# Kernel tuning notes

Measured on AMD Instinct MI355X. Metric: run time of the kernel, lower is better.

## Reference

```python
import jax, jax.numpy as jnp
import numpy as np

N_HEADS = 16
HEAD_DIM = 64
THRESHOLD = 0.5
TAU = 12.5
N_FHN_STEPS = 2


def fhn_imex_step(v, w, I, a, b, dt, tau):
    # IMEX step of FitzHugh-Nagumo dynamics:
    #   explicit update for v (nonlinear), implicit for w (linear in w)
    #   dv/dt = v - v^3/3 - w + I
    #   dw/dt = (v + a - b*w) / tau
    v_new = v + dt * (v - v ** 3 / 3.0 - w + I)
    w_new = (w + (dt / tau) * (v_new + a)) / (1.0 + (dt / tau) * b)
    return v_new, w_new


def setup_inputs() -> dict:
    key = jax.random.key(0)
    k1, k2, k3 = jax.random.split(key, 3)
    B, T, D = 2, 2048, 1024
    x = jax.random.normal(k1, (B, T, D), dtype=jnp.float32)
    Wqkv = jax.random.normal(k2, (3 * D, D), dtype=jnp.float32) * 0.02
    Wout = jax.random.normal(k3, (D, D), dtype=jnp.float32) * 0.02
    a = jnp.float32(0.7)
    b = jnp.float32(0.8)
    dt = jnp.float32(1.0)
    return {"x": x, "Wqkv": Wqkv, "Wout": Wout, "a": a, "b": b, "dt": dt}


def reference(x, Wqkv, Wout, a, b, dt):
    B, T, D = x.shape
    H, hd = N_HEADS, HEAD_DIM
    qkv = x @ Wqkv.T                              # (B, T, 3D)
    qkv = qkv.reshape(B, T, 3, H, hd)             # 'b t (three h d)'
    q = qkv[:, :, 0].transpose(0, 2, 1, 3)        # (B, H, T, hd)
    k = qkv[:, :, 1].transpose(0, 2, 1, 3)
    v = qkv[:, :, 2].transpose(0, 2, 1, 3)

    scores = jnp.einsum('bhtd,bhsd->bhts', q, k) / np.sqrt(hd).astype(np.float32)
    causal = jnp.triu(jnp.ones((T, T), dtype=bool), k=1)
    scores = jnp.where(causal[None, None], -jnp.inf, scores)
    attn_probs = jax.nn.softmax(scores, axis=-1)  # (B, H, T, T); dropout=0 -> identity

    attn_energy = attn_probs.sum(axis=-1)                              # (B, H, T)
    stim_scale = jnp.maximum(jnp.abs(attn_energy).max(axis=-1, keepdims=True), 1e-6)
    stimulus_normed = attn_energy / stim_scale
    threshold_gate = jax.nn.sigmoid((jnp.abs(attn_energy) - THRESHOLD) * 10.0)
    I = stimulus_normed * (0.1 + 0.9 * threshold_gate)                 # (B, H, T)
    I = jnp.broadcast_to(I[..., None], (B, H, T, hd))                  # expand to head_dim

    v_state = jnp.zeros_like(I)
    w_state = jnp.zeros_like(I)
    for _ in range(N_FHN_STEPS):
        v_state, w_state = fhn_imex_step(v_state, w_state, I, a, b, dt, TAU)

    fhn_gate = jax.nn.sigmoid(v_state.mean(axis=-1))[..., None]        # (B, H, T, 1)
    attn_probs = attn_probs * (0.5 + 0.5 * fhn_gate)
    attn_probs = attn_probs / (attn_probs.sum(axis=-1, keepdims=True) + 1e-8)

    out = jnp.einsum('bhts,bhsd->bhtd', attn_probs, v)                 # (B, H, T, hd)
    out = out.transpose(0, 2, 1, 3).reshape(B, T, D)
    out = out @ Wout.T
    return out
```

## Files before the change

### kernel.cpp

```cpp
#include <hip/hip_runtime.h>

typedef unsigned short u16;
typedef __attribute__((ext_vector_type(8))) short bf16x8;
typedef __attribute__((ext_vector_type(4))) float f32x4;
typedef __attribute__((ext_vector_type(4))) unsigned short u16x4;
typedef __attribute__((ext_vector_type(4))) unsigned int u32x4;

__device__ __forceinline__ u16 f2bf(float f) {
    unsigned int u = __builtin_bit_cast(unsigned int, f);
    u += 0x7fffu + ((u >> 16) & 1u);
    return (u16)(u >> 16);
}

__device__ __forceinline__ float bf2f(u16 b) {
    unsigned int u = ((unsigned int)b) << 16;
    return __builtin_bit_cast(float, u);
}

__device__ __forceinline__ unsigned int cvt_pk_bf16(float lo, float hi) {
    unsigned int r;
    asm("v_cvt_pk_bf16_f32 %0, %1, %2" : "=v"(r) : "v"(lo), "v"(hi));
    return r;
}

__device__ __forceinline__ void gload_lds16(const u16* g, const u16* l) {
    __builtin_amdgcn_global_load_lds((const __attribute__((address_space(1))) void*)g,
                                     (__attribute__((address_space(3))) void*)l,
                                     16, 0, 0);
}

__global__ __launch_bounds__(256) void cvt3_f32_bf16(const float* __restrict__ a, u16* __restrict__ ab, int na4,
                                                     const float* __restrict__ b, u16* __restrict__ bb, int nb4,
                                                     const float* __restrict__ c, u16* __restrict__ cb, int nc4) {
    const int stride = gridDim.x * blockDim.x;
    int i0 = blockIdx.x * blockDim.x + threadIdx.x;
    for (int i = i0; i < na4; i += stride) {
        float4 v = reinterpret_cast<const float4*>(a)[i];
        u16x4 o = { f2bf(v.x), f2bf(v.y), f2bf(v.z), f2bf(v.w) };
        reinterpret_cast<u16x4*>(ab)[i] = o;
    }
    for (int i = i0; i < nb4; i += stride) {
        float4 v = reinterpret_cast<const float4*>(b)[i];
        u16x4 o = { f2bf(v.x), f2bf(v.y), f2bf(v.z), f2bf(v.w) };
        reinterpret_cast<u16x4*>(bb)[i] = o;
    }
    for (int i = i0; i < nc4; i += stride) {
        float4 v = reinterpret_cast<const float4*>(c)[i];
        u16x4 o = { f2bf(v.x), f2bf(v.y), f2bf(v.z), f2bf(v.w) };
        reinterpret_cast<u16x4*>(cb)[i] = o;
    }
}

template <int BM, int BN, typename OutT>
__global__ __launch_bounds__(256) void gemm_bt(const u16* __restrict__ A, const u16* __restrict__ B,
                                               OutT* __restrict__ C, int M, int N, int K) {
    __shared__ u16 ldsA[BM * 64];
    __shared__ u16 ldsB[BN * 64];
    constexpr int RA = BM * 8 / 256;
    constexpr int RB = BN * 8 / 256;
    constexpr int MF = BM / 32;
    constexpr int NF = BN / 32;
    const int tid = threadIdx.x;
    const int lane = tid & 63;
    const int wid = tid >> 6;
    const int wm = wid >> 1, wn = wid & 1;
    const int lq = lane & 15, lg = lane >> 4;

    const int nbn = N / BN;
    const int id = blockIdx.x;
    const int idp = (id & 7) * ((int)gridDim.x >> 3) + (id >> 3);
    const int bm = (idp / nbn) * BM;
    const int bn = (idp % nbn) * BN;

    const u16* aSrc[RA];
    const u16* bSrc[RB];
    int dstOffA[RA], dstOffB[RB];
#pragma unroll
    for (int j = 0; j < RA; ++j) {
        int item = j * 256 + tid;
        aSrc[j] = A + (size_t)(bm + (item >> 3)) * K + (item & 7) * 8;
        dstOffA[j] = (j * 256 + (tid & ~63)) * 16;
    }
#pragma unroll
    for (int j = 0; j < RB; ++j) {
        int item = j * 256 + tid;
        bSrc[j] = B + (size_t)(bn + (item >> 3)) * K + (item & 7) * 8;
        dstOffB[j] = (j * 256 + (tid & ~63)) * 16;
    }

    f32x4 acc[MF][NF] = {};
    for (int k0 = 0; k0 < K; k0 += 64) {
        if (k0) __syncthreads();
#pragma unroll
        for (int j = 0; j < RA; ++j) {
            gload_lds16(aSrc[j], (const u16*)((const char*)ldsA + dstOffA[j]));
            aSrc[j] += 64;
        }
#pragma unroll
        for (int j = 0; j < RB; ++j) {
            gload_lds16(bSrc[j], (const u16*)((const char*)ldsB + dstOffB[j]));
            bSrc[j] += 64;
        }
        __syncthreads();
#pragma unroll
        for (int kk = 0; kk < 2; ++kk) {
            bf16x8 af[MF], bfr[NF];
#pragma unroll
            for (int m = 0; m < MF; ++m) {
                int row = wm * (BM / 2) + m * 16 + lq;
                af[m] = *(const bf16x8*)((const char*)ldsA + row * 128 + kk * 64 + lg * 16);
            }
#pragma unroll
            for (int n = 0; n < NF; ++n) {
                int row = wn * (BN / 2) + n * 16 + lq;
                bfr[n] = *(const bf16x8*)((const char*)ldsB + row * 128 + kk * 64 + lg * 16);
            }
#pragma unroll
            for (int m = 0; m < MF; ++m)
#pragma unroll
                for (int n = 0; n < NF; ++n)
                    acc[m][n] = __builtin_amdgcn_mfma_f32_16x16x32_bf16(af[m], bfr[n], acc[m][n], 0, 0, 0);
        }
    }

#pragma unroll
    for (int m = 0; m < MF; ++m) {
#pragma unroll
        for (int n = 0; n < NF; ++n) {
#pragma unroll
            for (int r = 0; r < 4; ++r) {
                int row = bm + wm * (BM / 2) + m * 16 + lg * 4 + r;
                int col = bn + wn * (BN / 2) + n * 16 + lq;
                float v = acc[m][n][r];
                if constexpr (sizeof(OutT) == 2)
                    C[(size_t)row * N + col] = (OutT)f2bf(v);
                else
                    C[(size_t)row * N + col] = (OutT)v;
            }
        }
    }
}

__global__ __launch_bounds__(256) void transpose_v(const u16* __restrict__ qkv, u16* __restrict__ vt) {
    __shared__ u16 tile[64][72];
    const int tb = blockIdx.x * 64;
    const int bh = blockIdx.y;
    const int b = bh >> 4, h = bh & 15;
    const u16* src = qkv + ((size_t)(b * 2048 + tb)) * 3072 + 2048 + h * 64;
    const int tid = threadIdx.x;
#pragma unroll
    for (int p = 0; p < 2; ++p) {
        int item = p * 256 + tid;
        int t = item >> 3, c = item & 7;
        bf16x8 v = *(const bf16x8*)(src + (size_t)t * 3072 + c * 8);
        *(bf16x8*)(&tile[t][c * 8]) = v;
    }
    __syncthreads();
    u16* dst = vt + ((size_t)bh * 64) * 2048 + tb;
#pragma unroll
    for (int p = 0; p < 2; ++p) {
        int item = p * 256 + tid;
        int d = item >> 3, tc = item & 7;
        bf16x8 o;
#pragma unroll
        for (int j = 0; j < 8; ++j) o[j] = (short)tile[tc * 8 + j][d];
        *(bf16x8*)(dst + (size_t)d * 2048 + tc * 8) = o;
    }
}

__global__ __launch_bounds__(256, 4) void fhn_attn(const u16* __restrict__ qkv, const u16* __restrict__ vt,
                                                   u16* __restrict__ attno,
                                                   u16* __restrict__ pO, float* __restrict__ pML) {
    __shared__ u16 kvbuf[2][2][64 * 64];
    const int id = blockIdx.x;
    const int xcd = id & 7;
    const int u = id >> 3;
    const int bh = xcd * 4 + (u & 3);
    const int unit = u >> 2;
    int qt, jb0, jb1, sidx;
    bool split;
    if (unit < 32) {
        qt = 31 - (unit >> 1);
        sidx = unit & 1;
        split = true;
        int n = qt + 1, hh = (n + 1) >> 1;
        jb0 = sidx ? hh : 0;
        jb1 = sidx ? n : hh;
    } else {
        qt = 47 - unit;
        sidx = 0;
        split = false;
        jb0 = 0;
        jb1 = qt + 1;
    }
    const int b = bh >> 4, h = bh & 15;
    const int tid = threadIdx.x;
    const int w = tid >> 6;
    const int lane = tid & 63;
    const int lq = lane & 15, lg = lane >> 4;
    const int qlo = qt * 64 + w * 16;
    const int tq = qlo + lq;

    bf16x8 qf[2];
    {
        const u16* qrow = qkv + ((size_t)(b * 2048 + tq)) * 3072 + h * 64;
        qf[0] = *(const bf16x8*)(qrow + lg * 8);
        qf[1] = *(const bf16x8*)(qrow + 32 + lg * 8);
#pragma unroll
        for (int kk = 0; kk < 2; ++kk)
#pragma unroll
            for (int j = 0; j < 8; ++j)
                qf[kk][j] = (short)f2bf(bf2f((u16)qf[kk][j]) * 0.1803368801f);
    }

    const int it0 = tid, it1 = 256 + tid;
    const int r0 = it0 >> 3, g0 = (it0 & 7) ^ (r0 & 7);
    const int r1 = it1 >> 3, g1 = (it1 & 7) ^ (r1 & 7);
    const int pr0 = (((r0 >> 4) & 1) << 5) | ((r0 & 12) << 1) | (((r0 >> 5) & 1) << 2) | (r0 & 3);
    const int pr1 = (((r1 >> 4) & 1) << 5) | ((r1 & 12) << 1) | (((r1 >> 5) & 1) << 2) | (r1 & 3);
    const u16* kS0 = qkv + ((size_t)(b * 2048 + jb0 * 64 + pr0)) * 3072 + 1024 + h * 64 + g0 * 8;
    const u16* kS1 = qkv + ((size_t)(b * 2048 + jb0 * 64 + pr1)) * 3072 + 1024 + h * 64 + g1 * 8;
    const u16* vS0 = vt + ((size_t)bh * 64 + r0) * 2048 + jb0 * 64 + g0 * 8;
    const u16* vS1 = vt + ((size_t)bh * 64 + r1) * 2048 + jb0 * 64 + g1 * 8;
    const int d0 = (it0 & ~63) * 8;
    const int d1 = (it1 & ~63) * 8;

#define STAGE(buf)                                            \
    do {                                                      \
        gload_lds16(kS0, &kvbuf[buf][0][d0]);                 \
        gload_lds16(kS1, &kvbuf[buf][0][d1]);                 \
        gload_lds16(vS0, &kvbuf[buf][1][d0]);                 \
        gload_lds16(vS1, &kvbuf[buf][1][d1]);                 \
        kS0 += 64 * 3072; kS1 += 64 * 3072;                   \
        vS0 += 64; vS1 += 64;                                 \
    } while (0)

    float m_run = -1e30f;
    f32x4 lacc = { 0.f, 0.f, 0.f, 0.f };
    f32x4 oacc[4] = {};
    int cur = 0;

    STAGE(0);

    for (int jb = jb0; jb < jb1; ++jb) {
        asm volatile("s_waitcnt vmcnt(0)" ::: "memory");
        __builtin_amdgcn_s_barrier();
        __builtin_amdgcn_sched_barrier(0);
        if (jb + 1 < jb1) STAGE(cur ^ 1);

        const u16* kb = kvbuf[cur][0];
        const u16* vb = kvbuf[cur][1];

        float p[4][4];
        __builtin_amdgcn_s_setprio(1);
#pragma unroll
        for (int st = 0; st < 4; ++st) {
            int row = st * 16 + lq;
            f32x4 sacc = {};
            sacc = __builtin_amdgcn_mfma_f32_16x16x32_bf16(
                *(const bf16x8*)(kb + row * 64 + ((lg ^ (row & 7)) * 8)), qf[0], sacc, 0, 0, 0);
            sacc = __builtin_amdgcn_mfma_f32_16x16x32_bf16(
                *(const bf16x8*)(kb + row * 64 + (((4 + lg) ^ (row & 7)) * 8)), qf[1], sacc, 0, 0, 0);
#pragma unroll
            for (int r = 0; r < 4; ++r) p[st][r] = sacc[r];
        }
        __builtin_amdgcn_s_setprio(0);

        bf16x8 vf[2][4];
#pragma unroll
        for (int c = 0; c < 2; ++c)
#pragma unroll
            for (int nd = 0; nd < 4; ++nd) {
                int row = nd * 16 + lq;
                vf[c][nd] = *(const bf16x8*)(vb + row * 64 + (((c * 4 + lg) ^ (row & 7)) * 8));
            }

        if (jb == qt) {
#pragma unroll
            for (int st = 0; st < 4; ++st)
#pragma unroll
                for (int r = 0; r < 4; ++r) {
                    int s = jb * 64 + ((st & 1) << 5) + (lg << 3) + ((st >> 1) << 2) + r;
                    if (s > tq) p[st][r] = -1e30f;
                }
        }

        float mst[4];
#pragma unroll
        for (int st = 0; st < 4; ++st)
            mst[st] = fmaxf(fmaxf(p[st][0], p[st][1]), fmaxf(p[st][2], p[st][3]));
        float mloc = fmaxf(fmaxf(mst[0], mst[1]), fmaxf(mst[2], mst[3]));
        mloc = fmaxf(mloc, __shfl_xor(mloc, 16));
        mloc = fmaxf(mloc, __shfl_xor(mloc, 32));

        if (!__all(mloc - m_run <= 8.0f)) {
            float mnew = fmaxf(m_run, mloc);
            float scp = exp2f(m_run - mnew);
            m_run = mnew;
#pragma unroll
            for (int st = 0; st < 4; ++st) lacc[st] *= scp;
            float f0 = __shfl(scp, lg * 4 + 0);
            float f1 = __shfl(scp, lg * 4 + 1);
            float f2_ = __shfl(scp, lg * 4 + 2);
            float f3 = __shfl(scp, lg * 4 + 3);
#pragma unroll
            for (int nd = 0; nd < 4; ++nd) {
                oacc[nd][0] *= f0; oacc[nd][1] *= f1;
                oacc[nd][2] *= f2_; oacc[nd][3] *= f3;
            }
        }

#pragma unroll
        for (int st = 0; st < 4; ++st) {
#pragma unroll
            for (int r = 0; r < 4; ++r)
                p[st][r] = exp2f(p[st][r] - m_run);
            lacc[st] += (p[st][0] + p[st][1]) + (p[st][2] + p[st][3]);
        }

        __builtin_amdgcn_s_setprio(1);
#pragma unroll
        for (int c = 0; c < 2; ++c) {
            u32x4 pw = { cvt_pk_bf16(p[c][0], p[c][1]),
                         cvt_pk_bf16(p[c][2], p[c][3]),
                         cvt_pk_bf16(p[c + 2][0], p[c + 2][1]),
                         cvt_pk_bf16(p[c + 2][2], p[c + 2][3]) };
            bf16x8 pa = __builtin_bit_cast(bf16x8, pw);
#pragma unroll
            for (int nd = 0; nd < 4; ++nd)
                oacc[nd] = __builtin_amdgcn_mfma_f32_16x16x32_bf16(pa, vf[c][nd], oacc[nd], 0, 0, 0);
        }
        __builtin_amdgcn_s_setprio(0);

        cur ^= 1;
    }
#undef STAGE

    float l_run = (lacc[0] + lacc[1]) + (lacc[2] + lacc[3]);
    l_run += __shfl_xor(l_run, 16);
    l_run += __shfl_xor(l_run, 32);

    if (split) {
        const int pidx = ((((bh << 4) | (qt - 16)) << 1) + sidx);
        u16* obase = pO + (size_t)pidx * 4096;
#pragma unroll
        for (int nd = 0; nd < 4; ++nd)
#pragma unroll
            for (int r = 0; r < 4; ++r) {
                int rt = w * 16 + lg * 4 + r;
                obase[rt * 64 + nd * 16 + lq] = f2bf(oacc[nd][r]);
            }
        if (lg == 0) {
            pML[pidx * 128 + w * 16 + lq] = m_run;
            pML[pidx * 128 + 64 + w * 16 + lq] = l_run;
        }
    } else {
        float li0 = 1.f / __shfl(l_run, lg * 4 + 0);
        float li1 = 1.f / __shfl(l_run, lg * 4 + 1);
        float li2 = 1.f / __shfl(l_run, lg * 4 + 2);
        float li3 = 1.f / __shfl(l_run, lg * 4 + 3);
#pragma unroll
        for (int nd = 0; nd < 4; ++nd) {
#pragma unroll
            for (int r = 0; r < 4; ++r) {
                int trow = qlo + lg * 4 + r;
                float li = (r == 0) ? li0 : (r == 1) ? li1 : (r == 2) ? li2 : li3;
                attno[((size_t)(b * 2048 + trow)) * 1024 + h * 64 + nd * 16 + lq] =
                    f2bf(oacc[nd][r] * li);
            }
        }
    }
}

__global__ __launch_bounds__(256) void attn_merge(const u16* __restrict__ pO, const float* __restrict__ pML,
                                                  u16* __restrict__ attno) {
    const int tilei = blockIdx.x;
    const int bh = tilei >> 4, q16 = tilei & 15;
    const int qt = 16 + q16;
    const int b = bh >> 4, h = bh & 15;
    const int p0 = tilei * 2, p1 = p0 + 1;
    const int t = threadIdx.x;
    const int rt = t >> 2;
    const int c0 = (t & 3) * 16;

    float m0 = pML[p0 * 128 + rt], l0 = pML[p0 * 128 + 64 + rt];
    float m1 = pML[p1 * 128 + rt], l1 = pML[p1 * 128 + 64 + rt];
    float M = fmaxf(m0, m1);
    float a0 = exp2f(m0 - M), a1 = exp2f(m1 - M);
    float inv = 1.f / (l0 * a0 + l1 * a1);
    a0 *= inv; a1 *= inv;

    const u16* O0 = pO + (size_t)p0 * 4096 + rt * 64 + c0;
    const u16* O1 = pO + (size_t)p1 * 4096 + rt * 64 + c0;
    u16* dst = attno + ((size_t)(b * 2048 + qt * 64 + rt)) * 1024 + h * 64 + c0;
#pragma unroll
    for (int half = 0; half < 2; ++half) {
        bf16x8 v0 = *(const bf16x8*)(O0 + half * 8);
        bf16x8 v1 = *(const bf16x8*)(O1 + half * 8);
        bf16x8 o;
#pragma unroll
        for (int j = 0; j < 8; ++j)
            o[j] = (short)f2bf(bf2f((u16)v0[j]) * a0 + bf2f((u16)v1[j]) * a1);
        *(bf16x8*)(dst + half * 8) = o;
    }
}

extern "C" void kernel_launch(void* const* d_in, const int* in_sizes, int n_in,
                              void* d_out, int out_size, void* d_ws, size_t ws_size,
                              hipStream_t stream) {
    const float* x    = (const float*)d_in[0];
    const float* Wqkv = (const float*)d_in[1];
    const float* Wout = (const float*)d_in[2];
    float* out = (float*)d_out;

    char* ws = (char*)d_ws;
    u16* xb    = (u16*)(ws + 0);
    u16* wqkvb = (u16*)(ws + 8388608);
    u16* woutb = (u16*)(ws + 14680064);
    u16* qkvb  = (u16*)(ws + 16777216);
    u16* vtb   = (u16*)(ws + 41943040);
    u16* attno = (u16*)(ws + 50331648);
    u16* pO    = xb;
    float* pML = (float*)wqkvb;

    cvt3_f32_bf16<<<2048, 256, 0, stream>>>(x, xb, 4194304 / 4,
                                            Wqkv, wqkvb, 3145728 / 4,
                                            Wout, woutb, 1048576 / 4);

    gemm_bt<128, 128, u16><<<768, 256, 0, stream>>>(xb, wqkvb, qkvb, 4096, 3072, 1024);

    transpose_v<<<dim3(32, 32), 256, 0, stream>>>(qkvb, vtb);

    fhn_attn<<<1536, 256, 0, stream>>>(qkvb, vtb, attno, pO, pML);

    attn_merge<<<512, 256, 0, stream>>>(pO, pML, attno);

    gemm_bt<64, 128, float><<<512, 256, 0, stream>>>(attno, woutb, out, 4096, 1024, 1024);
}
```

Measured before the change: 111.8 us.

## Add 4-stage async-LDS pipelined GEMM for QKV projection

Replaces the QKV projection GEMM with a new kernel that keeps a 4-deep ring of 32-wide K tiles in LDS, loaded directly from global memory to LDS with vmcnt-based waits, so loads for later tiles overlap MFMA work on the current one. It also remaps block IDs to group neighbouring tiles and raises wave priority around the MFMA burst. The aim is to hide global-load latency in the largest GEMM. In exchange it issues one barrier per K-step of 32, which doubles the barrier count, and it writes output with scalar stores that may not coalesce well.

New measurement: 114.3 us. 2.2% more time.

```diff
diff --git a/kernel.cpp b/kernel.cpp
--- a/kernel.cpp
+++ b/kernel.cpp
@@ -48,6 +48,102 @@
         float4 v = reinterpret_cast<const float4*>(c)[i];
         u16x4 o = { f2bf(v.x), f2bf(v.y), f2bf(v.z), f2bf(v.w) };
         reinterpret_cast<u16x4*>(cb)[i] = o;
+    }
+}
+
+template <typename OutT>
+__global__ __launch_bounds__(256) void gemm_bt_pipe(const u16* __restrict__ A, const u16* __restrict__ B,
+                                                    OutT* __restrict__ C, int M, int N, int K) {
+    __shared__ u16 lds[4][2][128 * 32];
+    const int tid = threadIdx.x;
+    const int lane = tid & 63;
+    const int wid = tid >> 6;
+    const int wm = wid >> 1, wn = wid & 1;
+    const int lq = lane & 15, lg = lane >> 4;
+
+    const int nbn = N >> 7;
+    const int id = blockIdx.x;
+    const int idp = (id & 7) * ((int)gridDim.x >> 3) + (id >> 3);
+    const int bm = (idp / nbn) * 128;
+    const int bn = (idp % nbn) * 128;
+
+    const u16* aS[2];
+    const u16* bS[2];
+    int dOff[2];
+#pragma unroll
+    for (int j = 0; j < 2; ++j) {
+        int idx = j * 256 + tid;
+        int row = idx >> 2, c16 = idx & 3;
+        aS[j] = A + (size_t)(bm + row) * K + c16 * 8;
+        bS[j] = B + (size_t)(bn + row) * K + c16 * 8;
+        dOff[j] = (j * 256 + (tid & ~63)) * 8;
+    }
+    int sb = 0;
+
+#define STAGE_T()                                              \
+    do {                                                       \
+        u16* la_ = &lds[sb][0][0];                             \
+        u16* lb_ = &lds[sb][1][0];                             \
+        gload_lds16(aS[0], la_ + dOff[0]);                     \
+        gload_lds16(aS[1], la_ + dOff[1]);                     \
+        gload_lds16(bS[0], lb_ + dOff[0]);                     \
+        gload_lds16(bS[1], lb_ + dOff[1]);                     \
+        aS[0] += 32; aS[1] += 32; bS[0] += 32; bS[1] += 32;    \
+        sb = (sb + 1) & 3;                                     \
+    } while (0)
+
+    const int nkt = K >> 5;
+    STAGE_T(); STAGE_T(); STAGE_T();
+
+    f32x4 acc[4][4] = {};
+    for (int kt = 0; kt < nkt; ++kt) {
+        if (kt < nkt - 2) {
+            asm volatile("s_waitcnt vmcnt(8)" ::: "memory");
+        } else if (kt == nkt - 2) {
+            asm volatile("s_waitcnt vmcnt(4)" ::: "memory");
+        } else {
+            asm volatile("s_waitcnt vmcnt(0)" ::: "memory");
+        }
+        __builtin_amdgcn_s_barrier();
+        __builtin_amdgcn_sched_barrier(0);
+        if (kt + 3 < nkt) STAGE_T();
+
+        const u16* la = &lds[kt & 3][0][0];
+        const u16* lb = &lds[kt & 3][1][0];
+        bf16x8 af[4], bfr[4];
+#pragma unroll
+        for (int m = 0; m < 4; ++m)
+            af[m] = *(const bf16x8*)(la + (wm * 64 + m * 16 + lq) * 32 + lg * 8);
+#pragma unroll
+        for (int n = 0; n < 4; ++n)
+            bfr[n] = *(const bf16x8*)(lb + (wn * 64 + n * 16 + lq) * 32 + lg * 8);
+        asm volatile("s_waitcnt lgkmcnt(0)" ::: "memory");
+        __builtin_amdgcn_sched_barrier(0);
+        __builtin_amdgcn_s_setprio(1);
+#pragma unroll
+        for (int m = 0; m < 4; ++m)
+#pragma unroll
+            for (int n = 0; n < 4; ++n)
+                acc[m][n] = __builtin_amdgcn_mfma_f32_16x16x32_bf16(af[m], bfr[n], acc[m][n], 0, 0, 0);
+        __builtin_amdgcn_s_setprio(0);
+    }
+#undef STAGE_T
+
+#pragma unroll
+    for (int m = 0; m < 4; ++m) {
+#pragma unroll
+        for (int n = 0; n < 4; ++n) {
+#pragma unroll
+            for (int r = 0; r < 4; ++r) {
+                int row = bm + wm * 64 + m * 16 + lg * 4 + r;
+                int col = bn + wn * 64 + n * 16 + lq;
+                float v = acc[m][n][r];
+                if constexpr (sizeof(OutT) == 2)
+                    C[(size_t)row * N + col] = (OutT)f2bf(v);
+                else
+                    C[(size_t)row * N + col] = (OutT)v;
+            }
+        }
     }
 }
 
@@ -427,7 +523,7 @@
                                             Wqkv, wqkvb, 3145728 / 4,
                                             Wout, woutb, 1048576 / 4);
 
-    gemm_bt<128, 128, u16><<<768, 256, 0, stream>>>(xb, wqkvb, qkvb, 4096, 3072, 1024);
+    gemm_bt_pipe<u16><<<768, 256, 0, stream>>>(xb, wqkvb, qkvb, 4096, 3072, 1024);
 
     transpose_v<<<dim3(32, 32), 256, 0, stream>>>(qkvb, vtb);
 
```
